# Performance work log

Measured on AMD Instinct MI355X. Metric: run time of the kernel, lower is better.

## Reference

```python
import jax, jax.numpy as jnp
import numpy as np
from math import factorial as _f

MAX_L = 2
NUM_CHANNELS = 64
B, N, C = 4, 1024, 64


def _cg_coeff(l1, m1, l2, m2, L, M):
    # Standard real Clebsch-Gordan coefficient <l1 m1 l2 m2 | L M> (Condon-Shortley)
    if m1 + m2 != M or not (abs(l1 - l2) <= L <= l1 + l2):
        return 0.0
    pre = ((2 * L + 1) * _f(L + l1 - l2) * _f(L - l1 + l2) * _f(l1 + l2 - L) / _f(l1 + l2 + L + 1)) ** 0.5
    pre *= (_f(L + M) * _f(L - M) * _f(l1 - m1) * _f(l1 + m1) * _f(l2 - m2) * _f(l2 + m2)) ** 0.5
    s = 0.0
    for k in range(0, l1 + l2 - L + 1):
        dens = [k, l1 + l2 - L - k, l1 - m1 - k, l2 + m2 - k, L - l2 + m1 + k, L - l1 - m2 + k]
        if any(d < 0 for d in dens):
            continue
        term = (-1.0) ** k
        for d in dens:
            term /= _f(d)
        s += term
    return pre * s


def _cg_tensor(l1, l2, L):
    # dense CG block [2l1+1, 2l2+1, 2L+1]
    T = np.zeros((2 * l1 + 1, 2 * l2 + 1, 2 * L + 1), np.float32)
    for i, m1 in enumerate(range(-l1, l1 + 1)):
        for j, m2 in enumerate(range(-l2, l2 + 1)):
            for k, M in enumerate(range(-L, L + 1)):
                T[i, j, k] = _cg_coeff(l1, m1, l2, m2, L, M)
    return jnp.asarray(T)


# precompute small CG blocks once (tiny, static)
_CG = {(l1, l2, L): _cg_tensor(l1, l2, L)
       for l1 in range(MAX_L + 1) for l2 in range(MAX_L + 1)
       for L in range(MAX_L + 1) if abs(l1 - l2) <= L <= l1 + l2}


def setup_inputs() -> dict:
    key = jax.random.key(0)
    ks = jax.random.split(key, 7)
    inp = {}
    for l, k in zip(range(MAX_L + 1), ks[:3]):
        inp[f"v{l}"] = jax.random.normal(k, (B, N, 2 * l + 1, C), jnp.float32)
    for l, k in zip(range(MAX_L + 1), ks[3:6]):
        inp[f"s{l}"] = jax.random.normal(k, (B, N, N, 2 * l + 1, 1), jnp.float32)
    inp["conn"] = jax.random.randint(ks[6], (B, N, N), 0, 2, jnp.int32)
    return inp


def reference(v0, v1, v2, s0, s1, s2, conn):
    v = [v0, v1, v2]
    sph = [s0, s1, s2]
    # sphx.parts[l] = einsum('bijmc->bimc', sph.parts[l]) : sum over neighbor index j
    sx = [jnp.einsum('bijmc->bimc', s) for s in sph]
    adj = conn.astype(v0.dtype)  # [B,N,N] gather mask (Rmask1)

    # CGproduct(vertices, sphx): for each output degree L, concat all (l1,l2) fragments
    cg_parts = []
    for L in range(MAX_L + 1):
        frags = []
        for l1 in range(MAX_L + 1):
            for l2 in range(MAX_L + 1):
                if abs(l1 - l2) <= L <= l1 + l2:
                    # [B,N,2L+1,C*1]
                    o = jnp.einsum('bnic,bnjd,ijk->bnkcd', v[l1], sx[l2], _CG[(l1, l2, L)])
                    frags.append(o.reshape(o.shape[0], o.shape[1], 2 * L + 1, -1))
        cg_parts.append(jnp.concatenate(frags, axis=-1))

    # message passing: sum-gather over connected neighbors
    mp = [jnp.einsum('bnm,bmkc->bnkc', adj, p) for p in cg_parts]

    # per-l normalization: divide by (2l+1)*||part||_F / num_channels
    normed = []
    for L, p in enumerate(mp):
        nf = (2 * L + 1) * jnp.linalg.norm(p)
        normed.append(p / (nf / NUM_CHANNELS))

    # flatten (m, channel) per degree and concat for a single output array
    return jnp.concatenate([p.reshape(p.shape[0], p.shape[1], -1) for p in normed], axis=-1)
```

## Files before the change

kernel.cpp:

```cpp
#include <hip/hip_runtime.h>
#include <math.h>

typedef __attribute__((ext_vector_type(8))) short short8;
typedef __attribute__((ext_vector_type(4))) float f32x4;

#define B_   4
#define N_   1024
#define FTOT 3264
#define FPAD 3328

#define WS_SS   0
#define WS_CG   256
#define WS_SX   4096
#define WS_ABF  151552
#define WS_PT   8540160

__device__ __forceinline__ unsigned short f2bf(float x) {
  union { float f; unsigned u; } v; v.f = x;
  unsigned r = v.u + 0x7FFFu + ((v.u >> 16) & 1u);
  return (unsigned short)(r >> 16);
}

__device__ __forceinline__ void gload16(const void* gp, void* lp) {
  __builtin_amdgcn_global_load_lds((const __attribute__((address_space(1))) unsigned int*)gp,
                                   (__attribute__((address_space(3))) unsigned int*)lp, 16, 0, 0);
}

__device__ __forceinline__ float wave_sum(float v) {
#pragma unroll
  for (int off = 32; off > 0; off >>= 1) v += __shfl_down(v, off, 64);
  return v;
}

__device__ double dfact(int n) { double r = 1.0; for (int i = 2; i <= n; ++i) r *= (double)i; return r; }

__device__ float cg_coeff(int l1, int m1, int l2, int m2, int L, int M) {
  if (m1 + m2 != M) return 0.f;
  int dl = l1 - l2; if (dl < 0) dl = -dl;
  if (L < dl || L > l1 + l2) return 0.f;
  double pre = sqrt((double)(2*L+1) * dfact(L+l1-l2) * dfact(L-l1+l2) * dfact(l1+l2-L) / dfact(l1+l2+L+1));
  pre *= sqrt(dfact(L+M)*dfact(L-M)*dfact(l1-m1)*dfact(l1+m1)*dfact(l2-m2)*dfact(l2+m2));
  double s = 0.0;
  for (int k = 0; k <= l1 + l2 - L; ++k) {
    int d1 = l1+l2-L-k, d2 = l1-m1-k, d3 = l2+m2-k, d4 = L-l2+m1+k, d5 = L-l1-m2+k;
    if (d1 < 0 || d2 < 0 || d3 < 0 || d4 < 0 || d5 < 0) continue;
    double t = (k & 1) ? -1.0 : 1.0;
    t /= dfact(k)*dfact(d1)*dfact(d2)*dfact(d3)*dfact(d4)*dfact(d5);
    s += t;
  }
  return (float)(pre * s);
}

__device__ const int t_l1[15]  = {0,1,2, 0,1,1,1,2,2, 0,1,1,2,2,2};
__device__ const int t_l2[15]  = {0,1,2, 1,0,1,2,1,2, 2,1,2,0,1,2};
__device__ const int t_L [15]  = {0,0,0, 1,1,1,1,1,1, 2,2,2,2,2,2};
__device__ const int t_off[16] = {0,1,10, 35,44,53,80,125,170, 245,270,315,390,415,490, 615};

__device__ const int d_l1[3][6]  = {{0,1,2,0,0,0},{0,1,1,1,2,2},{0,1,1,2,2,2}};
__device__ const int d_l2[3][6]  = {{0,1,2,0,0,0},{1,0,1,2,1,2},{2,1,2,0,1,2}};
__device__ const int d_off[3][6] = {{0,1,10,0,0,0},{35,44,53,80,125,170},{245,270,315,390,415,490}};
__device__ const int d_rb[3] = {0, 1, 4};

__global__ void k_init(float* ss, float* cg) {
  int tid = threadIdx.x;
  if (tid < 4) ss[tid] = 0.f;
  if (tid >= 615) return;
  int t = 0;
  while (t < 14 && tid >= t_off[t+1]) ++t;
  int local = tid - t_off[t];
  int l1 = t_l1[t], l2 = t_l2[t], L = t_L[t];
  int nk = 2*L+1, n2 = 2*l2+1;
  int k = local % nk; int rest = local / nk;
  int j = rest % n2;  int i = rest / n2;
  cg[tid] = cg_coeff(l1, i - l1, l2, j - l2, L, k - L);
}

__global__ __launch_bounds__(256) void k_sx(const float* __restrict__ s0p, const float* __restrict__ s1p,
                                            const float* __restrict__ s2p, float* __restrict__ sx) {
  __shared__ float red[9][256];
  const int bn = blockIdx.x;
  const int tid = threadIdx.x;
  const f32x4* p0 = (const f32x4*)(s0p + (size_t)bn * 1024);
  const f32x4* p1 = (const f32x4*)(s1p + (size_t)bn * 3072);
  const f32x4* p2 = (const f32x4*)(s2p + (size_t)bn * 5120);

  f32x4 va = p0[tid];
  f32x4 vb[3];
#pragma unroll
  for (int it = 0; it < 3; ++it) vb[it] = p1[tid + 256 * it];
  f32x4 vc[5];
#pragma unroll
  for (int it = 0; it < 5; ++it) vc[it] = p2[tid + 256 * it];

  float a = va[0] + va[1] + va[2] + va[3];

  float b[3] = {0.f, 0.f, 0.f};
#pragma unroll
  for (int it = 0; it < 3; ++it)
#pragma unroll
    for (int e = 0; e < 4; ++e)
      b[(it + e) % 3] += vb[it][e];

  float c[5] = {0.f, 0.f, 0.f, 0.f, 0.f};
#pragma unroll
  for (int it = 0; it < 5; ++it)
#pragma unroll
    for (int e = 0; e < 4; ++e)
      c[(4 * it + e) % 5] += vc[it][e];

  red[0][tid] = a;
  const int r3 = tid % 3;
#pragma unroll
  for (int u = 0; u < 3; ++u) red[1 + (r3 + u) % 3][tid] = b[u];
  const int q5 = (4 * tid) % 5;
#pragma unroll
  for (int u = 0; u < 5; ++u) red[4 + (q5 + u) % 5][tid] = c[u];
  __syncthreads();

  const int lane = tid & 63, w = tid >> 6;
  for (int r = w; r < 9; r += 4) {
    float v = red[r][lane] + red[r][lane + 64] + red[r][lane + 128] + red[r][lane + 192];
    v = wave_sum(v);
    if (lane == 0) sx[(size_t)bn * 9 + r] = v;
  }
}

__global__ __launch_bounds__(256) void k_adj(const int* __restrict__ conn, unsigned short* __restrict__ Abf) {
  const int idx  = blockIdx.x * 256 + threadIdx.x;
  const int lane = idx & 63;
  const int w    = (idx >> 6) & 2047;
  const int b    = idx >> 17;
  const int nt16 = w >> 5;
  const int ks   = w & 31;
  const int l16  = lane & 15, quad = lane >> 4;
  const int n    = nt16 * 16 + l16;
  const int m8   = ks * 32 + quad * 8;
  const int4* src = (const int4*)(conn + ((size_t)(b * 1024 + n) * 1024 + m8));
  int4 c0 = src[0], c1 = src[1];
  short8 o;
  o[0] = f2bf((float)c0.x); o[1] = f2bf((float)c0.y);
  o[2] = f2bf((float)c0.z); o[3] = f2bf((float)c0.w);
  o[4] = f2bf((float)c1.x); o[5] = f2bf((float)c1.y);
  o[6] = f2bf((float)c1.z); o[7] = f2bf((float)c1.w);
  const int nt = n >> 7, nr = n & 127;
  *(short8*)&Abf[(size_t)(b * 8 + nt) * 131072 + ks * 4096 +
                 ((nr >> 4) * 4 + quad) * 128 + (nr & 15) * 8] = o;
}

#define VSTRIDE 148

template <int L>
__device__ __forceinline__ void cg_emit(const float* __restrict__ vme, const float sxr[9],
                                        const float* __restrict__ cgt,
                                        unsigned short* __restrict__ pout, int cbase) {
  const int nfrag = (L == 0) ? 3 : 6;
  const int nk = 2 * L + 1;
  const int Lbase = (L == 0) ? 0 : (L == 1 ? 192 : 1344);
  const int Cfrag = nfrag * 64;
#pragma unroll
  for (int frag = 0; frag < nfrag; ++frag) {
    const int l1 = d_l1[L][frag], l2 = d_l2[L][frag];
    const int n1 = 2 * l1 + 1, n2 = 2 * l2 + 1;
    const int rb1 = d_rb[l1], rb2 = d_rb[l2];
    const int cgo = d_off[L][frag];
#pragma unroll
    for (int k = 0; k < nk; ++k) {
      float w[5];
#pragma unroll
      for (int i = 0; i < n1; ++i) {
        float a = 0.f;
#pragma unroll
        for (int j = 0; j < n2; ++j)
          a += sxr[rb2 + j] * cgt[cgo + (i * n2 + j) * nk + k];
        w[i] = a;
      }
      f32x4 val = {0.f, 0.f, 0.f, 0.f};
#pragma unroll
      for (int i = 0; i < n1; ++i) {
        f32x4 vv = *(const f32x4*)(vme + (rb1 + i) * 16);
        val += vv * w[i];
      }
      const int fb = Lbase + k * Cfrag + frag * 64 + cbase;
      const int ftile = fb >> 7, fr = fb & 127;
      unsigned short* pp = pout + (size_t)ftile * 131072 + (fr >> 4) * 512 + (fr & 15) * 8;
#pragma unroll
      for (int cc = 0; cc < 4; ++cc)
        pp[cc * 8] = f2bf(val[cc]);
    }
  }
}

__global__ __launch_bounds__(256) void k_cgp(const float* __restrict__ v0, const float* __restrict__ v1,
                                             const float* __restrict__ v2, const float* __restrict__ sx,
                                             const float* __restrict__ cgt, unsigned short* __restrict__ Pt) {
  __shared__ float vsh[64 * VSTRIDE];
  const int half = blockIdx.x & 1;
  const int cq   = blockIdx.x >> 1;
  const int mt   = blockIdx.y;
  const int b    = blockIdx.z;
  const int m0 = mt * 64;
  const int c0 = cq * 16;
  const int tid = threadIdx.x;
  const size_t nb = (size_t)b * N_ + m0;

  for (int e = tid; e < 9216; e += 256) {
    const int m = e / 144, rest = e % 144;
    const int r = rest >> 4, cc = rest & 15;
    float val;
    if (r == 0)      val = v0[(nb + m) * 64 + c0 + cc];
    else if (r < 4)  val = v1[((nb + m) * 3 + (r - 1)) * 64 + c0 + cc];
    else             val = v2[((nb + m) * 5 + (r - 4)) * 64 + c0 + cc];
    vsh[m * VSTRIDE + rest] = val;
  }
  const int lane = tid & 63, wv = tid >> 6;
  float sxr[9];
#pragma unroll
  for (int r = 0; r < 9; ++r) sxr[r] = sx[(nb + lane) * 9 + r];
  __syncthreads();

  const int ks = mt * 2 + (lane >> 5);
  const int kq = ((lane & 31) >> 3) * 128 + (lane & 7);
  unsigned short* pout = Pt + (size_t)b * 26 * 131072 + ks * 4096 + kq;
  const int cbase = c0 + wv * 4;
  const float* vme = &vsh[lane * VSTRIDE + wv * 4];

  if (half == 0) {
    cg_emit<0>(vme, sxr, cgt, pout, cbase);
    cg_emit<1>(vme, sxr, cgt, pout, cbase);
  } else {
    cg_emit<2>(vme, sxr, cgt, pout, cbase);
    const int fr = 64 + cbase;
    unsigned short* pp = pout + (size_t)25 * 131072 + (fr >> 4) * 512 + (fr & 15) * 8;
#pragma unroll
    for (int cc = 0; cc < 4; ++cc)
      pp[cc * 8] = 0;
  }
}

#define WAIT_VM8 0x0F78
#define WAIT_VM0 0x0F70

__global__ __launch_bounds__(512, 2) void k_gemm(const unsigned short* __restrict__ PtT,
                                                 const unsigned short* __restrict__ AbT,
                                                 float* __restrict__ out, float* __restrict__ ssv) {
  __shared__ unsigned short As[2][2][8192];
  __shared__ unsigned short Bs[2][2][8192];
  const int i  = blockIdx.x;
  const int x  = i & 7, j = i >> 3;
  const int b   = x >> 1;
  const int ntp = 2 * (x & 1) + (j & 1);
  const int ftp = j >> 1;
  const int f0 = ftp * 256, n0 = ntp * 256;
  const int tid  = threadIdx.x;
  const int w    = tid >> 6, lane = tid & 63;
  const int wr   = w >> 2, wc = w & 3;
  const int l16  = lane & 15, quad = lane >> 4;

  const unsigned short* gA0 = PtT + (size_t)(b * 26 + 2 * ftp    ) * 131072;
  const unsigned short* gA1 = PtT + (size_t)(b * 26 + 2 * ftp + 1) * 131072;
  const unsigned short* gB0 = AbT + (size_t)(b * 8  + 2 * ntp    ) * 131072;
  const unsigned short* gB1 = AbT + (size_t)(b * 8  + 2 * ntp + 1) * 131072;
  const int so = w * 512 + lane * 8;

#define ISSUE(T, BUF) do { \
    const size_t o = (size_t)(T) * 8192 + so; \
    gload16(gA0 + o,        &As[BUF][0][w * 512]); \
    gload16(gA0 + o + 4096, &As[BUF][0][4096 + w * 512]); \
    gload16(gA1 + o,        &As[BUF][1][w * 512]); \
    gload16(gA1 + o + 4096, &As[BUF][1][4096 + w * 512]); \
    gload16(gB0 + o,        &Bs[BUF][0][w * 512]); \
    gload16(gB0 + o + 4096, &Bs[BUF][0][4096 + w * 512]); \
    gload16(gB1 + o,        &Bs[BUF][1][w * 512]); \
    gload16(gB1 + o + 4096, &Bs[BUF][1][4096 + w * 512]); \
  } while (0)

  f32x4 acc[8][4] = {};
  const int bh  = wc >> 1;
  const int bl4 = (wc & 1) * 4;

#define COMPUTE(BUF) do { \
    _Pragma("unroll") \
    for (int kc = 0; kc < 2; ++kc) { \
      short8 bf[4]; \
      _Pragma("unroll") \
      for (int ni = 0; ni < 4; ++ni) \
        bf[ni] = *(const short8*)&Bs[BUF][bh][kc*4096 + ((bl4 + ni)*4 + quad)*128 + l16*8]; \
      _Pragma("unroll") \
      for (int mh = 0; mh < 2; ++mh) { \
        short8 af[4]; \
        _Pragma("unroll") \
        for (int m = 0; m < 4; ++m) \
          af[m] = *(const short8*)&As[BUF][wr][kc*4096 + ((mh*4 + m)*4 + quad)*128 + l16*8]; \
        _Pragma("unroll") \
        for (int m = 0; m < 4; ++m) \
          _Pragma("unroll") \
          for (int ni = 0; ni < 4; ++ni) \
            acc[mh*4 + m][ni] = __builtin_amdgcn_mfma_f32_16x16x32_bf16(af[m], bf[ni], acc[mh*4 + m][ni], 0, 0, 0); \
      } \
    } \
  } while (0)

  ISSUE(0, 0);
  ISSUE(1, 1);
  for (int t = 0; t < 15; ++t) {
    const int buf = t & 1;
    __builtin_amdgcn_s_waitcnt(WAIT_VM8);
    __builtin_amdgcn_s_barrier();
    COMPUTE(buf);
    __builtin_amdgcn_s_barrier();
    if (t < 14) ISSUE(t + 2, buf);
  }
  __builtin_amdgcn_s_waitcnt(WAIT_VM0);
  __builtin_amdgcn_s_barrier();
  COMPUTE(1);

  float ssl0 = 0.f, ssl1 = 0.f, ssl2 = 0.f;
#pragma unroll
  for (int mi = 0; mi < 8; ++mi) {
    const int fbase = f0 + wr*128 + mi*16 + quad*4;
    if (fbase >= FTOT) continue;
    float sq = 0.f;
#pragma unroll
    for (int ni = 0; ni < 4; ++ni) {
      const int n = n0 + wc*64 + ni*16 + l16;
      f32x4 v = acc[mi][ni];
      sq += v[0]*v[0] + v[1]*v[1] + v[2]*v[2] + v[3]*v[3];
      *(f32x4*)&out[((size_t)b * N_ + n) * FTOT + fbase] = v;
    }
    if (fbase < 192) ssl0 += sq; else if (fbase < 1344) ssl1 += sq; else ssl2 += sq;
  }
  ssl0 = wave_sum(ssl0); ssl1 = wave_sum(ssl1); ssl2 = wave_sum(ssl2);

  __syncthreads();
  float* red = (float*)&As[0][0][0];
  if (lane == 0) { red[w*3 + 0] = ssl0; red[w*3 + 1] = ssl1; red[w*3 + 2] = ssl2; }
  __syncthreads();
  if (tid < 3) {
    float s = 0.f;
#pragma unroll
    for (int ww = 0; ww < 8; ++ww) s += red[ww*3 + tid];
    if (s != 0.f) atomicAdd(&ssv[tid], s);
  }
#undef ISSUE
#undef COMPUTE
}

__global__ __launch_bounds__(256) void k_scale(float* __restrict__ out, const float* __restrict__ ssv) {
  const int idx = blockIdx.x * 256 + threadIdx.x;
  const int total = B_ * N_ * (FTOT / 4);
  if (idx >= total) return;
  const int f = (idx % (FTOT / 4)) * 4;
  const int L = f < 192 ? 0 : (f < 1344 ? 1 : 2);
  const float sc = 64.f / ((float)(2*L+1) * sqrtf(ssv[L]));
  f32x4* p = (f32x4*)out + idx;
  f32x4 v = *p;
  v *= sc;
  *p = v;
}

extern "C" void kernel_launch(void* const* d_in, const int* in_sizes, int n_in,
                              void* d_out, int out_size, void* d_ws, size_t ws_size,
                              hipStream_t stream) {
  const float* v0 = (const float*)d_in[0];
  const float* v1 = (const float*)d_in[1];
  const float* v2 = (const float*)d_in[2];
  const float* s0 = (const float*)d_in[3];
  const float* s1 = (const float*)d_in[4];
  const float* s2 = (const float*)d_in[5];
  const int* conn = (const int*)d_in[6];
  char* ws = (char*)d_ws;
  float* ss            = (float*)(ws + WS_SS);
  float* cg            = (float*)(ws + WS_CG);
  float* sx            = (float*)(ws + WS_SX);
  unsigned short* Abf  = (unsigned short*)(ws + WS_ABF);
  unsigned short* Pt   = (unsigned short*)(ws + WS_PT);
  float* out = (float*)d_out;

  k_init <<<dim3(1),            dim3(640), 0, stream>>>(ss, cg);
  k_sx   <<<dim3(B_ * N_),      dim3(256), 0, stream>>>(s0, s1, s2, sx);
  k_adj  <<<dim3(2048),         dim3(256), 0, stream>>>(conn, Abf);
  k_cgp  <<<dim3(8, 16, B_),    dim3(256), 0, stream>>>(v0, v1, v2, sx, cg, Pt);
  k_gemm <<<dim3(208),          dim3(512), 0, stream>>>(Pt, Abf, out, ss);
  k_scale<<<dim3(13056),        dim3(256), 0, stream>>>(out, ss);
}
```

Before: 297.8 us.

## Make k_sx persistent with double-buffered global-to-LDS async loads

The neighbour-sum kernel changes from one block per (b,n) row to 256 persistent blocks, each handling 16 rows. Each block double-buffers the s0/s1/s2 slices into LDS with global_load_lds, overlapping the fetch of row s+2 with the reduction of row s, and uses explicit vmcnt waits and barriers. The goal is to cut launch and tail overhead and keep the loads streaming through this bandwidth-bound reduction. The cost is a large LDS footprint (about 83KB per block), which allows only one block per CU. That lowers occupancy, so memory-level parallelism now depends on the two-stage pipeline.

```diff
diff --git a/kernel.cpp b/kernel.cpp
--- a/kernel.cpp
+++ b/kernel.cpp
@@ -75,54 +75,82 @@
   cg[tid] = cg_coeff(l1, i - l1, l2, j - l2, L, k - L);
 }
 
+#define SXWAIT_VM9 0x0F79
+#define SXWAIT_VM0 0x0F70
+
 __global__ __launch_bounds__(256) void k_sx(const float* __restrict__ s0p, const float* __restrict__ s1p,
                                             const float* __restrict__ s2p, float* __restrict__ sx) {
+  __shared__ float stage[2][9216];
   __shared__ float red[9][256];
-  const int bn = blockIdx.x;
+  const int g   = blockIdx.x;
+  const int bn0 = g * 16;
   const int tid = threadIdx.x;
-  const f32x4* p0 = (const f32x4*)(s0p + (size_t)bn * 1024);
-  const f32x4* p1 = (const f32x4*)(s1p + (size_t)bn * 3072);
-  const f32x4* p2 = (const f32x4*)(s2p + (size_t)bn * 5120);
-
-  f32x4 va = p0[tid];
-  f32x4 vb[3];
-#pragma unroll
-  for (int it = 0; it < 3; ++it) vb[it] = p1[tid + 256 * it];
-  f32x4 vc[5];
-#pragma unroll
-  for (int it = 0; it < 5; ++it) vc[it] = p2[tid + 256 * it];
-
-  float a = va[0] + va[1] + va[2] + va[3];
-
-  float b[3] = {0.f, 0.f, 0.f};
-#pragma unroll
-  for (int it = 0; it < 3; ++it)
-#pragma unroll
-    for (int e = 0; e < 4; ++e)
-      b[(it + e) % 3] += vb[it][e];
-
-  float c[5] = {0.f, 0.f, 0.f, 0.f, 0.f};
-#pragma unroll
-  for (int it = 0; it < 5; ++it)
-#pragma unroll
-    for (int e = 0; e < 4; ++e)
-      c[(4 * it + e) % 5] += vc[it][e];
-
-  red[0][tid] = a;
-  const int r3 = tid % 3;
-#pragma unroll
-  for (int u = 0; u < 3; ++u) red[1 + (r3 + u) % 3][tid] = b[u];
-  const int q5 = (4 * tid) % 5;
-#pragma unroll
-  for (int u = 0; u < 5; ++u) red[4 + (q5 + u) % 5][tid] = c[u];
-  __syncthreads();
-
   const int lane = tid & 63, w = tid >> 6;
-  for (int r = w; r < 9; r += 4) {
-    float v = red[r][lane] + red[r][lane + 64] + red[r][lane + 128] + red[r][lane + 192];
-    v = wave_sum(v);
-    if (lane == 0) sx[(size_t)bn * 9 + r] = v;
-  }
+
+#define SX_ISSUE(S, BUF) do { \
+    const char* g0 = (const char*)(s0p + (size_t)(bn0 + (S)) * 1024) + w * 1024 + lane * 16; \
+    const char* g1 = (const char*)(s1p + (size_t)(bn0 + (S)) * 3072) + w * 1024 + lane * 16; \
+    const char* g2 = (const char*)(s2p + (size_t)(bn0 + (S)) * 5120) + w * 1024 + lane * 16; \
+    char* lb = (char*)&stage[BUF][0] + w * 1024; \
+    gload16(g0,         lb); \
+    gload16(g1,         lb + 4096); \
+    gload16(g1 + 4096,  lb + 8192); \
+    gload16(g1 + 8192,  lb + 12288); \
+    gload16(g2,         lb + 16384); \
+    gload16(g2 + 4096,  lb + 20480); \
+    gload16(g2 + 8192,  lb + 24576); \
+    gload16(g2 + 12288, lb + 28672); \
+    gload16(g2 + 16384, lb + 32768); \
+  } while (0)
+
+  SX_ISSUE(0, 0);
+  SX_ISSUE(1, 1);
+  for (int s = 0; s < 16; ++s) {
+    const int buf = s & 1;
+    if (s < 15) __builtin_amdgcn_s_waitcnt(SXWAIT_VM9);
+    else        __builtin_amdgcn_s_waitcnt(SXWAIT_VM0);
+    __builtin_amdgcn_s_barrier();
+
+    const float* base = &stage[buf][0];
+    f32x4 va = *(const f32x4*)(base + tid * 4);
+    f32x4 vb[3];
+#pragma unroll
+    for (int it = 0; it < 3; ++it) vb[it] = *(const f32x4*)(base + 1024 + (tid + 256 * it) * 4);
+    f32x4 vc[5];
+#pragma unroll
+    for (int it = 0; it < 5; ++it) vc[it] = *(const f32x4*)(base + 4096 + (tid + 256 * it) * 4);
+
+    float a = va[0] + va[1] + va[2] + va[3];
+    float b[3] = {0.f, 0.f, 0.f};
+#pragma unroll
+    for (int it = 0; it < 3; ++it)
+#pragma unroll
+      for (int e = 0; e < 4; ++e)
+        b[(it + e) % 3] += vb[it][e];
+    float c[5] = {0.f, 0.f, 0.f, 0.f, 0.f};
+#pragma unroll
+    for (int it = 0; it < 5; ++it)
+#pragma unroll
+      for (int e = 0; e < 4; ++e)
+        c[(4 * it + e) % 5] += vc[it][e];
+
+    red[0][tid] = a;
+    const int r3 = tid % 3;
+#pragma unroll
+    for (int u = 0; u < 3; ++u) red[1 + (r3 + u) % 3][tid] = b[u];
+    const int q5 = (4 * tid) % 5;
+#pragma unroll
+    for (int u = 0; u < 5; ++u) red[4 + (q5 + u) % 5][tid] = c[u];
+    __builtin_amdgcn_s_barrier();
+
+    for (int r = w; r < 9; r += 4) {
+      float v = red[r][lane] + red[r][lane + 64] + red[r][lane + 128] + red[r][lane + 192];
+      v = wave_sum(v);
+      if (lane == 0) sx[(size_t)(bn0 + s) * 9 + r] = v;
+    }
+    if (s < 14) SX_ISSUE(s + 2, buf);
+  }
+#undef SX_ISSUE
 }
 
 __global__ __launch_bounds__(256) void k_adj(const int* __restrict__ conn, unsigned short* __restrict__ Abf) {
@@ -377,7 +405,7 @@
   float* out = (float*)d_out;
 
   k_init <<<dim3(1),            dim3(640), 0, stream>>>(ss, cg);
-  k_sx   <<<dim3(B_ * N_),      dim3(256), 0, stream>>>(s0, s1, s2, sx);
+  k_sx   <<<dim3(256),          dim3(256), 0, stream>>>(s0, s1, s2, sx);
   k_adj  <<<dim3(2048),         dim3(256), 0, stream>>>(conn, Abf);
   k_cgp  <<<dim3(8, 16, B_),    dim3(256), 0, stream>>>(v0, v1, v2, sx, cg, Pt);
   k_gemm <<<dim3(208),          dim3(512), 0, stream>>>(Pt, Abf, out, ss);
```

Result: slower. 306.2 us (+2.8%).
